# Performance work log

Hardware: AMD Instinct MI355X
Metric: run time of the kernel (lower is better)

The kernel has to match this reference:

```python
import jax, jax.numpy as jnp
import numpy as np

B = 32768
IN_DIM = 768
HIDDENS = [2048, 1024, 512]
EMBED_DIM = 128
NUM_EMB = 1024
DEPTH = 3


def setup_inputs() -> dict:
    key = jax.random.key(0)
    ks = jax.random.split(key, 20)
    d = {"x": jax.random.normal(ks[0], (B, IN_DIM), dtype=jnp.float32)}
    # Encoder: in -> h0 -> h1 -> h2 -> embed  (weights stored as [in, out])
    enc_dims = [IN_DIM] + HIDDENS + [EMBED_DIM]
    for i in range(4):
        fan_in = enc_dims[i]
        d[f"enc_W{i+1}"] = jax.random.normal(ks[1 + i], (enc_dims[i], enc_dims[i + 1]), dtype=jnp.float32) / np.sqrt(fan_in)
        d[f"enc_b{i+1}"] = jnp.zeros((enc_dims[i + 1],), dtype=jnp.float32)
    # Decoder: embed -> h0 -> h1 -> h2 -> in
    dec_dims = [EMBED_DIM] + HIDDENS + [IN_DIM]
    for i in range(4):
        fan_in = dec_dims[i]
        d[f"dec_W{i+1}"] = jax.random.normal(ks[5 + i], (dec_dims[i], dec_dims[i + 1]), dtype=jnp.float32) / np.sqrt(fan_in)
        d[f"dec_b{i+1}"] = jnp.zeros((dec_dims[i + 1],), dtype=jnp.float32)
    # Codebook (nn.Embedding weight, initialized ~ N(0,1) as in the module)
    d["codebook"] = jax.random.normal(ks[9], (NUM_EMB, EMBED_DIM), dtype=jnp.float32)
    return d


def _encoder(x, W1, b1, W2, b2, W3, b3, W4, b4):
    x = jax.nn.relu(x @ W1 + b1)
    x = jax.nn.relu(x @ W2 + b2)
    x = jax.nn.relu(x @ W3 + b3)
    return x @ W4 + b4


def _decoder(x, W1, b1, W2, b2, W3, b3, W4, b4):
    x = jax.nn.relu(x @ W1 + b1)
    x = jax.nn.relu(x @ W2 + b2)
    x = jax.nn.relu(x @ W3 + b3)
    return x @ W4 + b4


def reference(x,
              enc_W1, enc_b1, enc_W2, enc_b2, enc_W3, enc_b3, enc_W4, enc_b4,
              dec_W1, dec_b1, dec_W2, dec_b2, dec_W3, dec_b3, dec_W4, dec_b4,
              codebook):
    z = _encoder(x, enc_W1, enc_b1, enc_W2, enc_b2, enc_W3, enc_b3, enc_W4, enc_b4)
    z_det = jax.lax.stop_gradient(z)

    cb_sq = jnp.sum(codebook * codebook, axis=1)  # [K]
    residue = z_det
    z_hat = jnp.zeros_like(z_det)
    codes = []
    for _ in range(DEPTH):  # residual quantization loop
        # squared L2 distances [B, K]
        dist = (jnp.sum(residue * residue, axis=1, keepdims=True)
                + cb_sq
                - 2.0 * residue @ codebook.T)
        idx = jnp.argmin(dist, axis=1)          # [B]
        codes.append(idx)
        z_hat = z_hat + codebook[idx]           # gather codebook vectors
        residue = z_det - z_hat
    all_codes = jnp.stack(codes, axis=1)        # [B, DEPTH] int

    # straight-through estimator: forward uses z_hat, grad flows through z
    z_flow = z + jax.lax.stop_gradient(z_hat - z)
    x_recon = _decoder(z_flow, dec_W1, dec_b1, dec_W2, dec_b2, dec_W3, dec_b3, dec_W4, dec_b4)
    return (x_recon, all_codes)
```

## Files before the change

### kernel.cpp

```cpp
#include <hip/hip_runtime.h>

#define FLT_MAX_C 3.402823466e+38f

typedef __attribute__((ext_vector_type(8))) __bf16 bf16x8;
typedef __attribute__((ext_vector_type(4))) float f32x4;

static __device__ __forceinline__ ushort f2bf(float x) {
    union { float f; unsigned u; } v; v.f = x;
    unsigned r = (v.u + 0x7FFFu + ((v.u >> 16) & 1u)) >> 16;
    return (ushort)r;
}

template<bool RELU>
__device__ __forceinline__ void gemm_f32_dev(
    const float* __restrict__ A, const float* __restrict__ W,
    const float* __restrict__ bias, float* __restrict__ C, int K, int N)
{
    __shared__ float As[8][128];
    __shared__ float Bs[8][132];
    const int tid = threadIdx.x;
    const int bm = blockIdx.y << 7;
    const int bn = blockIdx.x << 7;

    const int la_row = tid >> 1;
    const int la_k   = (tid & 1) << 2;
    const int lb_row = tid >> 5;
    const int lb_col = (tid & 31) << 2;
    const int tm4 = (tid >> 4) << 2;
    const int tn4 = (tid & 15) << 2;

    float acc[8][8];
    #pragma unroll
    for (int i = 0; i < 8; ++i)
        #pragma unroll
        for (int j = 0; j < 8; ++j) acc[i][j] = 0.f;

    const float* aptr = A + (size_t)(bm + la_row) * K + la_k;
    const float* bptr = W + (size_t)lb_row * N + bn + lb_col;

    float4 av = *(const float4*)(aptr);
    float4 bv = *(const float4*)(bptr);

    for (int k0 = 0; k0 < K; k0 += 8) {
        __syncthreads();
        As[la_k + 0][la_row] = av.x;
        As[la_k + 1][la_row] = av.y;
        As[la_k + 2][la_row] = av.z;
        As[la_k + 3][la_row] = av.w;
        *(float4*)(&Bs[lb_row][lb_col]) = bv;
        __syncthreads();
        if (k0 + 8 < K) {
            av = *(const float4*)(aptr + k0 + 8);
            bv = *(const float4*)(bptr + (size_t)(k0 + 8) * N);
        }
        #pragma unroll
        for (int kk = 0; kk < 8; ++kk) {
            float a[8], b[8];
            *(float4*)(a)     = *(const float4*)(&As[kk][tm4]);
            *(float4*)(a + 4) = *(const float4*)(&As[kk][tm4 + 64]);
            *(float4*)(b)     = *(const float4*)(&Bs[kk][tn4]);
            *(float4*)(b + 4) = *(const float4*)(&Bs[kk][tn4 + 64]);
            #pragma unroll
            for (int i = 0; i < 8; ++i)
                #pragma unroll
                for (int j = 0; j < 8; ++j)
                    acc[i][j] = fmaf(a[i], b[j], acc[i][j]);
        }
    }

    float bv0[8];
    #pragma unroll
    for (int j = 0; j < 8; ++j)
        bv0[j] = bias[bn + tn4 + (j < 4 ? j : 60 + j)];

    #pragma unroll
    for (int i = 0; i < 8; ++i) {
        int row = bm + tm4 + (i < 4 ? i : 60 + i);
        float* cp = C + (size_t)row * N + bn + tn4;
        float4 v0, v1;
        v0.x = acc[i][0] + bv0[0]; v0.y = acc[i][1] + bv0[1];
        v0.z = acc[i][2] + bv0[2]; v0.w = acc[i][3] + bv0[3];
        v1.x = acc[i][4] + bv0[4]; v1.y = acc[i][5] + bv0[5];
        v1.z = acc[i][6] + bv0[6]; v1.w = acc[i][7] + bv0[7];
        if (RELU) {
            v0.x = fmaxf(v0.x, 0.f); v0.y = fmaxf(v0.y, 0.f);
            v0.z = fmaxf(v0.z, 0.f); v0.w = fmaxf(v0.w, 0.f);
            v1.x = fmaxf(v1.x, 0.f); v1.y = fmaxf(v1.y, 0.f);
            v1.z = fmaxf(v1.z, 0.f); v1.w = fmaxf(v1.w, 0.f);
        }
        *(float4*)(cp) = v0;
        *(float4*)(cp + 64) = v1;
    }
}

template<bool RELU>
__device__ __forceinline__ void gemm_f32_64_dev(
    const float* __restrict__ A, const float* __restrict__ W,
    const float* __restrict__ bias, float* __restrict__ C, int K, int N)
{
    __shared__ float As[16][64];
    __shared__ float Bs[16][132];
    const int tid = threadIdx.x;
    const int bm = blockIdx.y << 6;
    const int bn = blockIdx.x << 7;

    const int la_row = tid & 63;
    const int la_k   = (tid >> 6) << 2;
    const int lb_row = tid >> 5;
    const int lb_col = (tid & 31) << 2;
    const int tr = tid >> 4;
    const int tc = tid & 15;

    float acc[4][8];
    #pragma unroll
    for (int i = 0; i < 4; ++i)
        #pragma unroll
        for (int j = 0; j < 8; ++j) acc[i][j] = 0.f;

    const float* aptr = A + (size_t)(bm + la_row) * K + la_k;
    const float* bptr = W + (size_t)lb_row * N + bn + lb_col;

    float4 av = *(const float4*)(aptr);
    float4 bv0 = *(const float4*)(bptr);
    float4 bv1 = *(const float4*)(bptr + (size_t)8 * N);

    for (int k0 = 0; k0 < K; k0 += 16) {
        __syncthreads();
        As[la_k + 0][la_row] = av.x;
        As[la_k + 1][la_row] = av.y;
        As[la_k + 2][la_row] = av.z;
        As[la_k + 3][la_row] = av.w;
        *(float4*)(&Bs[lb_row][lb_col]) = bv0;
        *(float4*)(&Bs[lb_row + 8][lb_col]) = bv1;
        __syncthreads();
        if (k0 + 16 < K) {
            av  = *(const float4*)(aptr + k0 + 16);
            bv0 = *(const float4*)(bptr + (size_t)(k0 + 16) * N);
            bv1 = *(const float4*)(bptr + (size_t)(k0 + 24) * N);
        }
        #pragma unroll
        for (int kk = 0; kk < 16; ++kk) {
            float a[4], b[8];
            *(float4*)(a) = *(const float4*)(&As[kk][tr << 2]);
            *(float4*)(b)     = *(const float4*)(&Bs[kk][tc << 2]);
            *(float4*)(b + 4) = *(const float4*)(&Bs[kk][(tc << 2) + 64]);
            #pragma unroll
            for (int i = 0; i < 4; ++i)
                #pragma unroll
                for (int j = 0; j < 8; ++j)
                    acc[i][j] = fmaf(a[i], b[j], acc[i][j]);
        }
    }

    float bb[8];
    #pragma unroll
    for (int j = 0; j < 8; ++j)
        bb[j] = bias[bn + (tc << 2) + (j < 4 ? j : 60 + j)];

    #pragma unroll
    for (int i = 0; i < 4; ++i) {
        float* cp = C + (size_t)(bm + (tr << 2) + i) * N + bn + (tc << 2);
        float4 v0, v1;
        v0.x = acc[i][0] + bb[0]; v0.y = acc[i][1] + bb[1];
        v0.z = acc[i][2] + bb[2]; v0.w = acc[i][3] + bb[3];
        v1.x = acc[i][4] + bb[4]; v1.y = acc[i][5] + bb[5];
        v1.z = acc[i][6] + bb[6]; v1.w = acc[i][7] + bb[7];
        if (RELU) {
            v0.x = fmaxf(v0.x, 0.f); v0.y = fmaxf(v0.y, 0.f);
            v0.z = fmaxf(v0.z, 0.f); v0.w = fmaxf(v0.w, 0.f);
            v1.x = fmaxf(v1.x, 0.f); v1.y = fmaxf(v1.y, 0.f);
            v1.z = fmaxf(v1.z, 0.f); v1.w = fmaxf(v1.w, 0.f);
        }
        *(float4*)(cp) = v0;
        *(float4*)(cp + 64) = v1;
    }
}

template<bool RELU, bool OUTF32>
__device__ __forceinline__ void gemm_bf16_dev(
    const ushort* __restrict__ A, const ushort* __restrict__ Wt,
    const float* __restrict__ bias, void* __restrict__ C, int K, int N)
{
    __shared__ __align__(16) ushort As[128][64];
    __shared__ __align__(16) ushort Bs[128][64];
    const int tid  = threadIdx.x;
    const int lane = tid & 63;
    const int wv   = tid >> 6;
    const int wm   = (wv >> 1) << 6;
    const int wn   = (wv & 1) << 6;
    const int bm   = blockIdx.y << 7;
    const int bn   = blockIdx.x << 7;
    const int lr   = lane & 15;
    const int lh   = lane >> 4;

    f32x4 acc[4][4];
    #pragma unroll
    for (int m = 0; m < 4; ++m)
        #pragma unroll
        for (int n = 0; n < 4; ++n) acc[m][n] = (f32x4){0.f, 0.f, 0.f, 0.f};

    for (int k0 = 0; k0 < K; k0 += 64) {
        __syncthreads();
        #pragma unroll
        for (int i = 0; i < 4; ++i) {
            const int c    = wv * 4 + i;
            const int boff = c * 1024 + lane * 16;
            const int r    = boff >> 7;
            const int cbt  = boff & 127;
            const char* sa = (const char*)A  + (((size_t)(bm + r) * K + k0) << 1) + cbt;
            const char* sb = (const char*)Wt + (((size_t)(bn + r) * K + k0) << 1) + cbt;
            __builtin_amdgcn_global_load_lds((const void*)sa, (void*)(&As[0][0] + c * 512), 16, 0, 0);
            __builtin_amdgcn_global_load_lds((const void*)sb, (void*)(&Bs[0][0] + c * 512), 16, 0, 0);
        }
        __syncthreads();
        #pragma unroll
        for (int kk = 0; kk < 64; kk += 32) {
            bf16x8 af[4], bfr[4];
            #pragma unroll
            for (int m = 0; m < 4; ++m)
                af[m] = *(const bf16x8*)&As[wm + m * 16 + lr][kk + lh * 8];
            #pragma unroll
            for (int n = 0; n < 4; ++n)
                bfr[n] = *(const bf16x8*)&Bs[wn + n * 16 + lr][kk + lh * 8];
            #pragma unroll
            for (int m = 0; m < 4; ++m)
                #pragma unroll
                for (int n = 0; n < 4; ++n)
                    acc[m][n] = __builtin_amdgcn_mfma_f32_16x16x32_bf16(
                        af[m], bfr[n], acc[m][n], 0, 0, 0);
        }
    }

    #pragma unroll
    for (int n = 0; n < 4; ++n) {
        const int col = bn + wn + n * 16 + lr;
        const float bcol = bias[col];
        #pragma unroll
        for (int m = 0; m < 4; ++m) {
            #pragma unroll
            for (int i = 0; i < 4; ++i) {
                const int row = bm + wm + m * 16 + lh * 4 + i;
                float v = acc[m][n][i] + bcol;
                if (RELU) v = fmaxf(v, 0.f);
                if (OUTF32) ((float*)C)[(size_t)row * N + col] = v;
                else        ((ushort*)C)[(size_t)row * N + col] = f2bf(v);
            }
        }
    }
}

__global__ __launch_bounds__(256) void enc1_gemm(const float* A, const float* W, const float* b, float* C)
{ gemm_f32_dev<true>(A, W, b, C, 768, 2048); }
__global__ __launch_bounds__(256) void enc2_gemm(const float* A, const float* W, const float* b, float* C)
{ gemm_f32_dev<true>(A, W, b, C, 2048, 1024); }
__global__ __launch_bounds__(256) void enc3_gemm(const float* A, const float* W, const float* b, float* C)
{ gemm_f32_dev<true>(A, W, b, C, 1024, 512); }
__global__ __launch_bounds__(256) void enc4_gemm(const float* A, const float* W, const float* b, float* C)
{ gemm_f32_64_dev<false>(A, W, b, C, 512, 128); }
__global__ __launch_bounds__(256) void dec1_gemm(const ushort* A, const ushort* Wt, const float* b, void* C)
{ gemm_bf16_dev<true, false>(A, Wt, b, C, 128, 2048); }
__global__ __launch_bounds__(256) void dec2_gemm(const ushort* A, const ushort* Wt, const float* b, void* C)
{ gemm_bf16_dev<true, false>(A, Wt, b, C, 2048, 1024); }
__global__ __launch_bounds__(256) void dec3_gemm(const ushort* A, const ushort* Wt, const float* b, void* C)
{ gemm_bf16_dev<true, false>(A, Wt, b, C, 1024, 512); }
__global__ __launch_bounds__(256) void dec4_gemm(const ushort* A, const ushort* Wt, const float* b, void* C)
{ gemm_bf16_dev<false, true>(A, Wt, b, C, 512, 768); }

__global__ __launch_bounds__(256) void wt_convert(
    const float* __restrict__ W, ushort* __restrict__ Wt, int K, int N)
{
    __shared__ ushort t[64][65];
    const int kb = blockIdx.y << 6, nb = blockIdx.x << 6;
    const int c  = threadIdx.x & 63;
    const int r0 = (threadIdx.x >> 6) << 4;
    #pragma unroll
    for (int i = 0; i < 16; ++i)
        t[r0 + i][c] = f2bf(W[(size_t)(kb + r0 + i) * N + nb + c]);
    __syncthreads();
    #pragma unroll
    for (int i = 0; i < 16; ++i)
        Wt[(size_t)(nb + r0 + i) * K + kb + c] = t[c][r0 + i];
}

__global__ __launch_bounds__(256) void cbsq_kernel(
    const float* __restrict__ cb, float* __restrict__ cbsq)
{
    int k = blockIdx.x * 256 + threadIdx.x;
    const float* r = cb + ((size_t)k << 7);
    float s = 0.f;
    #pragma unroll 8
    for (int d = 0; d < 128; ++d) s = fmaf(r[d], r[d], s);
    cbsq[k] = s;
}

__global__ __launch_bounds__(256) void cbt_kernel(
    const float* __restrict__ cb, float* __restrict__ cbt)
{
    __shared__ float t[64][65];
    const int kb = blockIdx.x << 6;
    const int db = blockIdx.y << 6;
    const int c  = threadIdx.x & 63;
    const int r0 = (threadIdx.x >> 6) << 4;
    #pragma unroll
    for (int i = 0; i < 16; ++i)
        t[r0 + i][c] = cb[(size_t)(kb + r0 + i) * 128 + db + c];
    __syncthreads();
    #pragma unroll
    for (int i = 0; i < 16; ++i)
        cbt[(size_t)(db + r0 + i) * 1024 + kb + c] = t[c][r0 + i];
}

__global__ __launch_bounds__(256) void rq_all(
    const float* __restrict__ z, const float* __restrict__ cbt,
    const float* __restrict__ sq, const float* __restrict__ cb,
    ushort* __restrict__ ZHb, float* __restrict__ codes)
{
    __shared__ float As[128][68];
    __shared__ float Bs[32][132];
    __shared__ float sqs[1024];
    __shared__ float rrs[64];

    const int tid = threadIdx.x;
    const int bm  = blockIdx.x << 6;
    const int tr  = tid >> 4;
    const int c   = tid & 15;
    const int tn4 = c << 2;
    const int lb_row = tid >> 5;
    const int lb_col = (tid & 31) << 2;

    #pragma unroll
    for (int i = 0; i < 4; ++i) sqs[tid + (i << 8)] = sq[tid + (i << 8)];

    float zh[4][8];
    #pragma unroll
    for (int i = 0; i < 4; ++i) {
        const int r_  = (tr << 2) + i;
        const float* zp = z + (size_t)(bm + r_) * 128 + (c << 3);
        float4 z0 = *(const float4*)(zp);
        float4 z1 = *(const float4*)(zp + 4);
        #pragma unroll
        for (int j = 0; j < 8; ++j) zh[i][j] = 0.f;
        As[(c << 3) + 0][r_] = z0.x; As[(c << 3) + 1][r_] = z0.y;
        As[(c << 3) + 2][r_] = z0.z; As[(c << 3) + 3][r_] = z0.w;
        As[(c << 3) + 4][r_] = z1.x; As[(c << 3) + 5][r_] = z1.y;
        As[(c << 3) + 6][r_] = z1.z; As[(c << 3) + 7][r_] = z1.w;
        float p = z0.x * z0.x;
        p = fmaf(z0.y, z0.y, p); p = fmaf(z0.z, z0.z, p);
        p = fmaf(z0.w, z0.w, p); p = fmaf(z1.x, z1.x, p);
        p = fmaf(z1.y, z1.y, p); p = fmaf(z1.z, z1.z, p);
        p = fmaf(z1.w, z1.w, p);
        #pragma unroll
        for (int o = 8; o >= 1; o >>= 1) p += __shfl_xor(p, o);
        if (c == 0) rrs[r_] = p;
    }
    __syncthreads();

    for (int t = 0; t < 3; ++t) {
        float rr_[4];
        #pragma unroll
        for (int i = 0; i < 4; ++i) rr_[i] = rrs[(tr << 2) + i];

        float best_d[4] = {FLT_MAX_C, FLT_MAX_C, FLT_MAX_C, FLT_MAX_C};
        int   best_i[4] = {0, 0, 0, 0};

        for (int bx = 0; bx < 8; ++bx) {
            const int bn = bx << 7;
            const float* bptr = cbt + (size_t)lb_row * 1024 + bn + lb_col;
            float4 bv0 = *(const float4*)(bptr);
            float4 bv1 = *(const float4*)(bptr + (size_t)8  * 1024);
            float4 bv2 = *(const float4*)(bptr + (size_t)16 * 1024);
            float4 bv3 = *(const float4*)(bptr + (size_t)24 * 1024);

            float acc[4][8];
            #pragma unroll
            for (int i = 0; i < 4; ++i)
                #pragma unroll
                for (int j = 0; j < 8; ++j) acc[i][j] = 0.f;

            for (int k0 = 0; k0 < 128; k0 += 32) {
                __syncthreads();
                *(float4*)(&Bs[lb_row +  0][lb_col]) = bv0;
                *(float4*)(&Bs[lb_row +  8][lb_col]) = bv1;
                *(float4*)(&Bs[lb_row + 16][lb_col]) = bv2;
                *(float4*)(&Bs[lb_row + 24][lb_col]) = bv3;
                __syncthreads();
                if (k0 + 32 < 128) {
                    bv0 = *(const float4*)(bptr + (size_t)(k0 + 32) * 1024);
                    bv1 = *(const float4*)(bptr + (size_t)(k0 + 40) * 1024);
                    bv2 = *(const float4*)(bptr + (size_t)(k0 + 48) * 1024);
                    bv3 = *(const float4*)(bptr + (size_t)(k0 + 56) * 1024);
                }
                #pragma unroll
                for (int kk = 0; kk < 32; ++kk) {
                    float a[4], b[8];
                    *(float4*)(a)     = *(const float4*)(&As[k0 + kk][tr << 2]);
                    *(float4*)(b)     = *(const float4*)(&Bs[kk][tn4]);
                    *(float4*)(b + 4) = *(const float4*)(&Bs[kk][tn4 + 64]);
                    #pragma unroll
                    for (int i = 0; i < 4; ++i)
                        #pragma unroll
                        for (int j = 0; j < 8; ++j)
                            acc[i][j] = fmaf(a[i], b[j], acc[i][j]);
                }
            }
            #pragma unroll
            for (int i = 0; i < 4; ++i) {
                #pragma unroll
                for (int j = 0; j < 8; ++j) {
                    const int col = bn + tn4 + (j < 4 ? j : 60 + j);
                    float d = (rr_[i] + sqs[col]) - 2.f * acc[i][j];
                    if (d < best_d[i]) { best_d[i] = d; best_i[i] = col; }
                }
            }
        }

        #pragma unroll
        for (int i = 0; i < 4; ++i) {
            float bd = best_d[i]; int bi = best_i[i];
            #pragma unroll
            for (int o = 8; o >= 1; o >>= 1) {
                float od = __shfl_xor(bd, o);
                int   oi = __shfl_xor(bi, o);
                if (od < bd || (od == bd && oi < bi)) { bd = od; bi = oi; }
            }
            best_i[i] = bi;
        }

        __syncthreads();

        #pragma unroll
        for (int i = 0; i < 4; ++i) {
            const int r_  = (tr << 2) + i;
            const int row = bm + r_;
            if (c == 0) codes[(size_t)row * 3 + t] = (float)best_i[i];

            const float* cbp = cb + ((size_t)best_i[i] << 7) + (c << 3);
            float4 c0 = *(const float4*)(cbp);
            float4 c1 = *(const float4*)(cbp + 4);
            zh[i][0] += c0.x; zh[i][1] += c0.y;
            zh[i][2] += c0.z; zh[i][3] += c0.w;
            zh[i][4] += c1.x; zh[i][5] += c1.y;
            zh[i][6] += c1.z; zh[i][7] += c1.w;

            if (t < 2) {
                const float* zp = z + (size_t)row * 128 + (c << 3);
                float4 z0 = *(const float4*)(zp);
                float4 z1 = *(const float4*)(zp + 4);
                float r0 = z0.x - zh[i][0], r1 = z0.y - zh[i][1];
                float r2 = z0.z - zh[i][2], r3 = z0.w - zh[i][3];
                float r4 = z1.x - zh[i][4], r5 = z1.y - zh[i][5];
                float r6 = z1.z - zh[i][6], r7 = z1.w - zh[i][7];
                As[(c << 3) + 0][r_] = r0; As[(c << 3) + 1][r_] = r1;
                As[(c << 3) + 2][r_] = r2; As[(c << 3) + 3][r_] = r3;
                As[(c << 3) + 4][r_] = r4; As[(c << 3) + 5][r_] = r5;
                As[(c << 3) + 6][r_] = r6; As[(c << 3) + 7][r_] = r7;
                float p = r0 * r0;
                p = fmaf(r1, r1, p); p = fmaf(r2, r2, p);
                p = fmaf(r3, r3, p); p = fmaf(r4, r4, p);
                p = fmaf(r5, r5, p); p = fmaf(r6, r6, p);
                p = fmaf(r7, r7, p);
                #pragma unroll
                for (int o = 8; o >= 1; o >>= 1) p += __shfl_xor(p, o);
                if (c == 0) rrs[r_] = p;
            } else {
                ushort4 o0, o1;
                o0.x = f2bf(zh[i][0]); o0.y = f2bf(zh[i][1]);
                o0.z = f2bf(zh[i][2]); o0.w = f2bf(zh[i][3]);
                o1.x = f2bf(zh[i][4]); o1.y = f2bf(zh[i][5]);
                o1.z = f2bf(zh[i][6]); o1.w = f2bf(zh[i][7]);
                ushort* zbp = ZHb + (size_t)row * 128 + (c << 3);
                *(ushort4*)(zbp)     = o0;
                *(ushort4*)(zbp + 4) = o1;
            }
        }
        if (t < 2) __syncthreads();
    }
}

extern "C" void kernel_launch(void* const* d_in, const int* in_sizes, int n_in,
                              void* d_out, int out_size, void* d_ws, size_t ws_size,
                              hipStream_t stream)
{
    const float* x   = (const float*)d_in[0];
    const float* eW1 = (const float*)d_in[1];
    const float* eb1 = (const float*)d_in[2];
    const float* eW2 = (const float*)d_in[3];
    const float* eb2 = (const float*)d_in[4];
    const float* eW3 = (const float*)d_in[5];
    const float* eb3 = (const float*)d_in[6];
    const float* eW4 = (const float*)d_in[7];
    const float* eb4 = (const float*)d_in[8];
    const float* dW1 = (const float*)d_in[9];
    const float* db1 = (const float*)d_in[10];
    const float* dW2 = (const float*)d_in[11];
    const float* db2 = (const float*)d_in[12];
    const float* dW3 = (const float*)d_in[13];
    const float* db3 = (const float*)d_in[14];
    const float* dW4 = (const float*)d_in[15];
    const float* db4 = (const float*)d_in[16];
    const float* cb  = (const float*)d_in[17];

    float* out   = (float*)d_out;
    float* codes = out + (size_t)32768 * 768;

    ushort* Wt1 = (ushort*)d_ws;
    ushort* Wt2 = Wt1 + (size_t)2048 * 128;
    ushort* Wt3 = Wt2 + (size_t)1024 * 2048;
    ushort* Wt4 = Wt3 + (size_t)512 * 1024;
    float*  sq  = (float*)(Wt4 + (size_t)768 * 512);
    float*  cbt = sq + 1024;
    float*  act = cbt + (size_t)128 * 1024;
    const size_t fixed_b = (char*)act - (char*)d_ws;

    int mc = 32768;
    while (mc > 1024) {
        if (fixed_b + (size_t)mc * 15104 <= ws_size) break;
        mc >>= 1;
    }

    float*  R1  = act;
    float*  R2  = R1 + (size_t)mc * 2048;
    float*  R3  = R2 + (size_t)mc * 1024;
    float*  RZ  = R3 + (size_t)mc * 512;
    ushort* ZHb = (ushort*)(RZ + (size_t)mc * 128);
    ushort* D1  = (ushort*)R1;
    ushort* D2  = (ushort*)R2;
    ushort* D3  = (ushort*)R3;

    wt_convert<<<dim3(2048 / 64, 128 / 64), 256, 0, stream>>>(dW1, Wt1, 128, 2048);
    wt_convert<<<dim3(1024 / 64, 2048 / 64), 256, 0, stream>>>(dW2, Wt2, 2048, 1024);
    wt_convert<<<dim3(512 / 64, 1024 / 64), 256, 0, stream>>>(dW3, Wt3, 1024, 512);
    wt_convert<<<dim3(768 / 64, 512 / 64), 256, 0, stream>>>(dW4, Wt4, 512, 768);
    cbsq_kernel<<<4, 256, 0, stream>>>(cb, sq);
    cbt_kernel<<<dim3(16, 2), 256, 0, stream>>>(cb, cbt);

    const int mg = mc >> 7;
    for (int r0 = 0; r0 < 32768; r0 += mc) {
        const float* xi     = x     + (size_t)r0 * 768;
        float*       outi   = out   + (size_t)r0 * 768;
        float*       codesi = codes + (size_t)r0 * 3;
        enc1_gemm<<<dim3(16, mg), 256, 0, stream>>>(xi, eW1, eb1, R1);
        enc2_gemm<<<dim3( 8, mg), 256, 0, stream>>>(R1, eW2, eb2, R2);
        enc3_gemm<<<dim3( 4, mg), 256, 0, stream>>>(R2, eW3, eb3, R3);
        enc4_gemm<<<dim3( 1, mc >> 6), 256, 0, stream>>>(R3, eW4, eb4, RZ);
        rq_all<<<mc >> 6, 256, 0, stream>>>(RZ, cbt, sq, cb, ZHb, codesi);
        dec1_gemm<<<dim3(16, mg), 256, 0, stream>>>(ZHb, Wt1, db1, D1);
        dec2_gemm<<<dim3( 8, mg), 256, 0, stream>>>(D1,  Wt2, db2, D2);
        dec3_gemm<<<dim3( 4, mg), 256, 0, stream>>>(D2,  Wt3, db3, D3);
        dec4_gemm<<<dim3( 6, mg), 256, 0, stream>>>(D3,  Wt4, db4, outi);
    }
}
```

Measured before the change: 3.923 ms.

## Fuse weight and codebook prep kernels, split encoder GEMMs into quarters

Merges the four weight transpose/convert kernels plus the codebook norm and transpose kernels into one prep_all launch, with the work picked per block index, to cut launch overhead. The first two encoder GEMMs are also issued as four launches, each covering a quarter of the rows. Since these launches run back to back on the same stream, the split adds launches and shrinks each grid rather than creating overlap. It may be meant to change cache behaviour, but it risks more overhead and lower occupancy per launch.

```diff
diff --git a/kernel.cpp b/kernel.cpp
--- a/kernel.cpp
+++ b/kernel.cpp
@@ -266,11 +266,12 @@
 __global__ __launch_bounds__(256) void dec4_gemm(const ushort* A, const ushort* Wt, const float* b, void* C)
 { gemm_bf16_dev<false, true>(A, Wt, b, C, 512, 768); }
 
-__global__ __launch_bounds__(256) void wt_convert(
-    const float* __restrict__ W, ushort* __restrict__ Wt, int K, int N)
-{
-    __shared__ ushort t[64][65];
-    const int kb = blockIdx.y << 6, nb = blockIdx.x << 6;
+__device__ __forceinline__ void wt_convert_dev(
+    const float* __restrict__ W, ushort* __restrict__ Wt, int K, int N,
+    int bx, int by, void* smem)
+{
+    ushort (*t)[65] = (ushort(*)[65])smem;
+    const int kb = by << 6, nb = bx << 6;
     const int c  = threadIdx.x & 63;
     const int r0 = (threadIdx.x >> 6) << 4;
     #pragma unroll
@@ -282,32 +283,44 @@
         Wt[(size_t)(nb + r0 + i) * K + kb + c] = t[c][r0 + i];
 }
 
-__global__ __launch_bounds__(256) void cbsq_kernel(
-    const float* __restrict__ cb, float* __restrict__ cbsq)
-{
-    int k = blockIdx.x * 256 + threadIdx.x;
-    const float* r = cb + ((size_t)k << 7);
-    float s = 0.f;
-    #pragma unroll 8
-    for (int d = 0; d < 128; ++d) s = fmaf(r[d], r[d], s);
-    cbsq[k] = s;
-}
-
-__global__ __launch_bounds__(256) void cbt_kernel(
-    const float* __restrict__ cb, float* __restrict__ cbt)
-{
-    __shared__ float t[64][65];
-    const int kb = blockIdx.x << 6;
-    const int db = blockIdx.y << 6;
-    const int c  = threadIdx.x & 63;
-    const int r0 = (threadIdx.x >> 6) << 4;
-    #pragma unroll
-    for (int i = 0; i < 16; ++i)
-        t[r0 + i][c] = cb[(size_t)(kb + r0 + i) * 128 + db + c];
-    __syncthreads();
-    #pragma unroll
-    for (int i = 0; i < 16; ++i)
-        cbt[(size_t)(db + r0 + i) * 1024 + kb + c] = t[c][r0 + i];
+__global__ __launch_bounds__(256) void prep_all(
+    const float* dW1, const float* dW2, const float* dW3, const float* dW4,
+    ushort* Wt1, ushort* Wt2, ushort* Wt3, ushort* Wt4,
+    const float* cb, float* sq, float* cbt)
+{
+    __shared__ float smem[64][65];
+    int b = blockIdx.x;
+    if (b < 64)  { wt_convert_dev(dW1, Wt1, 128,  2048, b % 32, b / 32, smem); return; }
+    b -= 64;
+    if (b < 512) { wt_convert_dev(dW2, Wt2, 2048, 1024, b % 16, b / 16, smem); return; }
+    b -= 512;
+    if (b < 128) { wt_convert_dev(dW3, Wt3, 1024, 512,  b % 8,  b / 8,  smem); return; }
+    b -= 128;
+    if (b < 96)  { wt_convert_dev(dW4, Wt4, 512,  768,  b % 12, b / 12, smem); return; }
+    b -= 96;
+    if (b < 4) {
+        int k = b * 256 + threadIdx.x;
+        const float* r = cb + ((size_t)k << 7);
+        float s = 0.f;
+        #pragma unroll 8
+        for (int d = 0; d < 128; ++d) s = fmaf(r[d], r[d], s);
+        sq[k] = s;
+        return;
+    }
+    b -= 4;
+    {
+        const int kb = (b % 16) << 6;
+        const int db = (b / 16) << 6;
+        const int c  = threadIdx.x & 63;
+        const int r0 = (threadIdx.x >> 6) << 4;
+        #pragma unroll
+        for (int i = 0; i < 16; ++i)
+            smem[r0 + i][c] = cb[(size_t)(kb + r0 + i) * 128 + db + c];
+        __syncthreads();
+        #pragma unroll
+        for (int i = 0; i < 16; ++i)
+            cbt[(size_t)(db + r0 + i) * 1024 + kb + c] = smem[c][r0 + i];
+    }
 }
 
 __global__ __launch_bounds__(256) void rq_all(
@@ -527,20 +540,22 @@
     ushort* D2  = (ushort*)R2;
     ushort* D3  = (ushort*)R3;
 
-    wt_convert<<<dim3(2048 / 64, 128 / 64), 256, 0, stream>>>(dW1, Wt1, 128, 2048);
-    wt_convert<<<dim3(1024 / 64, 2048 / 64), 256, 0, stream>>>(dW2, Wt2, 2048, 1024);
-    wt_convert<<<dim3(512 / 64, 1024 / 64), 256, 0, stream>>>(dW3, Wt3, 1024, 512);
-    wt_convert<<<dim3(768 / 64, 512 / 64), 256, 0, stream>>>(dW4, Wt4, 512, 768);
-    cbsq_kernel<<<4, 256, 0, stream>>>(cb, sq);
-    cbt_kernel<<<dim3(16, 2), 256, 0, stream>>>(cb, cbt);
+    prep_all<<<836, 256, 0, stream>>>(dW1, dW2, dW3, dW4, Wt1, Wt2, Wt3, Wt4,
+                                      cb, sq, cbt);
 
     const int mg = mc >> 7;
+    const int mq = mc >> 2;
+    const int mgq = mq >> 7;
     for (int r0 = 0; r0 < 32768; r0 += mc) {
         const float* xi     = x     + (size_t)r0 * 768;
         float*       outi   = out   + (size_t)r0 * 768;
         float*       codesi = codes + (size_t)r0 * 3;
-        enc1_gemm<<<dim3(16, mg), 256, 0, stream>>>(xi, eW1, eb1, R1);
-        enc2_gemm<<<dim3( 8, mg), 256, 0, stream>>>(R1, eW2, eb2, R2);
+        for (int q = 0; q < 4; ++q)
+            enc1_gemm<<<dim3(16, mgq), 256, 0, stream>>>(
+                xi + (size_t)q * mq * 768, eW1, eb1, R1 + (size_t)q * mq * 2048);
+        for (int q = 0; q < 4; ++q)
+            enc2_gemm<<<dim3(8, mgq), 256, 0, stream>>>(
+                R1 + (size_t)q * mq * 2048, eW2, eb2, R2 + (size_t)q * mq * 1024);
         enc3_gemm<<<dim3( 4, mg), 256, 0, stream>>>(R2, eW3, eb3, R3);
         enc4_gemm<<<dim3( 1, mc >> 6), 256, 0, stream>>>(R3, eW4, eb4, RZ);
         rq_all<<<mc >> 6, 256, 0, stream>>>(RZ, cbt, sq, cb, ZHb, codesi);
```

After: 4.420 ms. 12.7% more time.
